# Kernel optimization log

Hardware: AMD Instinct MI355X
Metric: run time of the kernel (lower is better)

The kernel has to match this reference:

```python
import jax, jax.numpy as jnp
import numpy as np
import math

SIZE = 11
PAD = 5
C1 = 0.01 ** 2
C2 = 0.03 ** 2


def gaussian_window():
    # Matches torch __init__: 1D gaussian (sigma=1.5), normalized, outer product,
    # expanded to depthwise weight of shape (3, 1, 11, 11)
    x = np.arange(SIZE, dtype=np.float32)
    g = np.exp(-((x - SIZE // 2) ** 2) / (2.0 * 1.5 ** 2)).astype(np.float32)
    g = g / g.sum()
    w2d = np.outer(g, g).astype(np.float32)  # (11, 11)
    return jnp.asarray(np.broadcast_to(w2d, (3, 1, SIZE, SIZE)).copy())


def depthwise_conv(x, win):
    return jax.lax.conv_general_dilated(
        x, win,
        window_strides=(1, 1),
        padding=[(PAD, PAD), (PAD, PAD)],
        dimension_numbers=('NCHW', 'OIHW', 'NCHW'),
        feature_group_count=3,
    )


def setup_inputs() -> dict:
    key = jax.random.key(0)
    k1, k2 = jax.random.split(key)
    img1 = jax.random.uniform(k1, (16, 3, 512, 512), dtype=jnp.float32)
    img2 = jax.random.uniform(k2, (16, 3, 512, 512), dtype=jnp.float32)
    return {"img1": img1, "img2": img2, "win": gaussian_window()}


def reference(img1, img2, win):
    mu1 = depthwise_conv(img1, win)
    mu2 = depthwise_conv(img2, win)
    mu1_sq = mu1 * mu1
    mu2_sq = mu2 * mu2
    mu1_mu2 = mu1 * mu2
    sig1_sq = depthwise_conv(img1 * img1, win) - mu1_sq
    sig2_sq = depthwise_conv(img2 * img2, win) - mu2_sq
    sig12 = depthwise_conv(img1 * img2, win) - mu1_mu2
    v = ((2.0 * mu1_mu2 + C1) * (2.0 * sig12 + C2)) / (
        (mu1_sq + mu2_sq + C1) * (sig1_sq + sig2_sq + C2))
    return 1.0 - jnp.mean(v)
```

## Files before the change

kernel.cpp:

```cpp
#include <hip/hip_runtime.h>


#define IMG 512
#define NPIX (16LL * 3 * 512 * 512)
#define GX 8
#define GY 4
#define NG 8
#define NBLK (GX * GY * 48)
#define NPART NBLK

typedef short v8s __attribute__((ext_vector_type(8)));
typedef float v4f __attribute__((ext_vector_type(4)));
typedef __bf16 bf2 __attribute__((ext_vector_type(2)));
typedef float f2  __attribute__((ext_vector_type(2)));

static __device__ __forceinline__ int cvtpk2(f2 v) {
    bf2 r = __builtin_convertvector(v, bf2);
    return __builtin_bit_cast(int, r);
}
static __device__ __forceinline__ unsigned f2bf(float f) {
    unsigned u = __float_as_uint(f);
    return (u + 0x7FFFu + ((u >> 16) & 1u)) >> 16;
}

static __device__ __forceinline__ void gload16(const float* g, void* lds) {
    __builtin_amdgcn_global_load_lds(
        (const __attribute__((address_space(1))) void*)g,
        (__attribute__((address_space(3))) void*)lds, 16, 0, 0);
}

template <int N>
static __device__ __forceinline__ void vwait() {
    if constexpr (N == 8)      asm volatile("s_waitcnt vmcnt(8)" ::: "memory");
    else if constexpr (N == 4) asm volatile("s_waitcnt vmcnt(4)" ::: "memory");
    else                       asm volatile("s_waitcnt vmcnt(0)" ::: "memory");
    __builtin_amdgcn_sched_barrier(0);
}

static __device__ __forceinline__ void h_rt(
    const float4 (&L)[4], v8s band, short (*hw)[16][40], int lm, int quad, int slot)
{
    const v4f zacc = {0.f, 0.f, 0.f, 0.f};
    const float4 a0 = L[0], a1 = L[1], b0 = L[2], b1 = L[3];
    f2 a0l; a0l.x = a0.x; a0l.y = a0.y;   f2 a0h; a0h.x = a0.z; a0h.y = a0.w;
    f2 a1l; a1l.x = a1.x; a1l.y = a1.y;   f2 a1h; a1h.x = a1.z; a1h.y = a1.w;
    f2 b0l; b0l.x = b0.x; b0l.y = b0.y;   f2 b0h; b0h.x = b0.z; b0h.y = b0.w;
    f2 b1l; b1l.x = b1.x; b1l.y = b1.y;   f2 b1h; b1h.x = b1.z; b1h.y = b1.w;

    v8s A[4]; int4 w;
    w.x = cvtpk2(a0l); w.y = cvtpk2(a0h); w.z = cvtpk2(a1l); w.w = cvtpk2(a1h);
    A[0] = __builtin_bit_cast(v8s, w);
    w.x = cvtpk2(b0l); w.y = cvtpk2(b0h); w.z = cvtpk2(b1l); w.w = cvtpk2(b1h);
    A[1] = __builtin_bit_cast(v8s, w);
    w.x = cvtpk2(__builtin_elementwise_fma(a0l, a0l, b0l * b0l));
    w.y = cvtpk2(__builtin_elementwise_fma(a0h, a0h, b0h * b0h));
    w.z = cvtpk2(__builtin_elementwise_fma(a1l, a1l, b1l * b1l));
    w.w = cvtpk2(__builtin_elementwise_fma(a1h, a1h, b1h * b1h));
    A[2] = __builtin_bit_cast(v8s, w);
    w.x = cvtpk2(a0l * b0l); w.y = cvtpk2(a0h * b0h);
    w.z = cvtpk2(a1l * b1l); w.w = cvtpk2(a1h * b1h);
    A[3] = __builtin_bit_cast(v8s, w);

    #pragma unroll
    for (int p = 0; p < 4; ++p) {
        const v4f acc = __builtin_amdgcn_mfma_f32_16x16x32_bf16(A[p], band, zacc, 0, 0, 0);
        int2 w2;
        f2 lo; lo.x = acc[0]; lo.y = acc[1];
        f2 hi; hi.x = acc[2]; hi.y = acc[3];
        w2.x = cvtpk2(lo); w2.y = cvtpk2(hi);
        *(int2*)&hw[p][lm][slot * 16 + quad * 4] = w2;
    }
}

static __device__ __forceinline__ void v_t2(
    v8s band, short (*hw)[16][40], int lm, int quad, int o, f2& vsum)
{
    const v4f zacc = {0.f, 0.f, 0.f, 0.f};
    const int bs = (quad * 8 + o * 16) & 31;
    v4f acc[4];
    #pragma unroll
    for (int p = 0; p < 4; ++p) {
        const v8s hf = *(const v8s*)&hw[p][lm][bs];
        acc[p] = __builtin_amdgcn_mfma_f32_16x16x32_bf16(band, hf, zacc, 0, 0, 0);
    }
    const f2 C1v = {1e-4f, 1e-4f};
    const f2 C2v = {9e-4f, 9e-4f};
    const f2 two = {2.f, 2.f};
    #pragma unroll
    for (int h = 0; h < 2; ++h) {
        f2 m1; m1.x = acc[0][2 * h]; m1.y = acc[0][2 * h + 1];
        f2 m2; m2.x = acc[1][2 * h]; m2.y = acc[1][2 * h + 1];
        f2 es; es.x = acc[2][2 * h]; es.y = acc[2][2 * h + 1];
        f2 ex; ex.x = acc[3][2 * h]; ex.y = acc[3][2 * h + 1];
        const f2 m1s = m1 * m1, m2s = m2 * m2, m12 = m1 * m2;
        const f2 sig = es - m1s - m2s;
        const f2 s12 = ex - m12;
        const f2 num = __builtin_elementwise_fma(two, m12, C1v) *
                       __builtin_elementwise_fma(two, s12, C2v);
        const f2 den = (m1s + m2s + C1v) * (sig + C2v);
        f2 r; r.x = __builtin_amdgcn_rcpf(den.x); r.y = __builtin_amdgcn_rcpf(den.y);
        vsum = __builtin_elementwise_fma(num, r, vsum);
    }
}

__global__ __launch_bounds__(256, 2) void ssim_kernel(
    const float* __restrict__ img1,
    const float* __restrict__ img2,
    const float* __restrict__ win,
    float* __restrict__ partial)
{
    __shared__ __align__(16) short hb[4][4][16][40];
    __shared__ __align__(16) float4 raw[4][3][4][64];

    const int tid  = threadIdx.x;
    const int lane = tid & 63;
    const int wave = tid >> 6;
    const int lm   = lane & 15;
    const int quad = lane >> 4;

    const int bx = blockIdx.x, by = blockIdx.y, z = blockIdx.z;
    const int rowbase = by * (NG * 16);

    float gl = 0.f;
    if (lane < 11) gl = win[55 + lane] * rsqrtf(win[60]);
    v8s band;
    #pragma unroll
    for (int j = 0; j < 8; ++j) {
        const int t  = quad * 8 + j - lm - 3;
        const int tc = ((unsigned)t > 10u) ? 11 : t;
        band[j] = (short)f2bf(__shfl(gl, tc));
    }

    const size_t zoff = (size_t)z * IMG * IMG;
    const float* p1 = img1 + zoff;
    const float* p2 = img2 + zoff;

    const int gct = bx * 4 + wave;
    const bool colOK = (gct > 0) & (gct < 31);
    const int gcol = gct * 16 - 8 + quad * 8;
    const int  colA = gcol < 0 ? 0 : (gcol > IMG - 4 ? IMG - 4 : gcol);
    const int  colB = (gcol + 4) < 0 ? 0 : ((gcol + 4) > IMG - 4 ? IMG - 4 : (gcol + 4));
    const bool cbA  = (unsigned)gcol >= (unsigned)IMG;
    const bool cbB  = (unsigned)(gcol + 4) >= (unsigned)IMG;
    const bool topE = (by == 0), botE = (by == GY - 1);
    short (*hw)[16][40] = hb[wave];

    auto issue_g = [&](int k, int slot) {
        const int gr  = rowbase + k * 16 - 8 + lm;
        const int grc = gr < 0 ? 0 : (gr > IMG - 1 ? IMG - 1 : gr);
        const float* r1 = p1 + (size_t)grc * IMG;
        const float* r2 = p2 + (size_t)grc * IMG;
        gload16(r1 + colA, &raw[wave][slot][0][0]);
        gload16(r1 + colB, &raw[wave][slot][1][0]);
        gload16(r2 + colA, &raw[wave][slot][2][0]);
        gload16(r2 + colB, &raw[wave][slot][3][0]);
    };
    auto consume_h = [&](int k, int slot) {
        float4 L[4];
        L[0] = raw[wave][slot][0][lane];
        L[1] = raw[wave][slot][1][lane];
        L[2] = raw[wave][slot][2][lane];
        L[3] = raw[wave][slot][3][lane];
        const bool rowsE = (k == 0 && topE) || (k == NG && botE);
        if (!colOK || rowsE) {
            const int gr = rowbase + k * 16 - 8 + lm;
            const bool rbad = (unsigned)gr >= (unsigned)IMG;
            float4 zz; zz.x = zz.y = zz.z = zz.w = 0.f;
            if (rbad | cbA) { L[0] = zz; L[2] = zz; }
            if (rbad | cbB) { L[1] = zz; L[3] = zz; }
        }
        h_rt(L, band, hw, lm, quad, k & 1);
    };

    f2 vsum = {0.f, 0.f};
    issue_g(0, 0); issue_g(1, 1); issue_g(2, 2);
    vwait<8>(); consume_h(0, 0);
    issue_g(3, 0); vwait<8>(); consume_h(1, 1); v_t2(band, hw, lm, quad, 0, vsum);
    issue_g(4, 1); vwait<8>(); consume_h(2, 2); v_t2(band, hw, lm, quad, 1, vsum);
    issue_g(5, 2); vwait<8>(); consume_h(3, 0); v_t2(band, hw, lm, quad, 2, vsum);
    issue_g(6, 0); vwait<8>(); consume_h(4, 1); v_t2(band, hw, lm, quad, 3, vsum);
    issue_g(7, 1); vwait<8>(); consume_h(5, 2); v_t2(band, hw, lm, quad, 4, vsum);
    issue_g(8, 2); vwait<8>(); consume_h(6, 0); v_t2(band, hw, lm, quad, 5, vsum);
                   vwait<4>(); consume_h(7, 1); v_t2(band, hw, lm, quad, 6, vsum);
                   vwait<0>(); consume_h(8, 2); v_t2(band, hw, lm, quad, 7, vsum);

    float vs = vsum.x + vsum.y;
    #pragma unroll
    for (int off = 32; off > 0; off >>= 1)
        vs += __shfl_down(vs, off, 64);
    if (lane == 0) *(float*)&hb[wave][3][15][36] = vs;
    __syncthreads();
    if (tid == 0) {
        float t = 0.f;
        #pragma unroll
        for (int w = 0; w < 4; ++w) t += *(const float*)&hb[w][3][15][36];
        partial[(z * GY + by) * GX + bx] = t;
    }
}

__global__ __launch_bounds__(512) void finalize_kernel(
    const float* __restrict__ partial, float* __restrict__ out)
{
    __shared__ float red[8];
    float s = 0.f;
    if (threadIdx.x < NPART / 4) {
        const float4 t = ((const float4*)partial)[threadIdx.x];
        s = (t.x + t.y) + (t.z + t.w);
    }
    #pragma unroll
    for (int off = 32; off > 0; off >>= 1)
        s += __shfl_down(s, off, 64);
    if ((threadIdx.x & 63) == 0) red[threadIdx.x >> 6] = s;
    __syncthreads();
    if (threadIdx.x == 0) {
        float t = 0.f;
        #pragma unroll
        for (int i = 0; i < 8; ++i) t += red[i];
        out[0] = 1.0f - t / (float)NPIX;
    }
}

extern "C" void kernel_launch(void* const* d_in, const int* in_sizes, int n_in,
                              void* d_out, int out_size, void* d_ws, size_t ws_size,
                              hipStream_t stream) {
    const float* img1 = (const float*)d_in[0];
    const float* img2 = (const float*)d_in[1];
    const float* win  = (const float*)d_in[2];
    float* partialb = (float*)d_ws;

    dim3 grid(GX, GY, 48);
    ssim_kernel<<<grid, dim3(256), 0, stream>>>(img1, img2, win, partialb);
    finalize_kernel<<<1, dim3(512), 0, stream>>>(partialb, (float*)d_out);
}
```

Before: 136.8 us.

## Double-buffer global-to-LDS loads, lengthen row strips, and raise occupancy

Each block now covers 256 rows instead of 128 (GY 2, NG 16). This halves the redundant 16-row halo loads per strip. The triple-buffered raw LDS staging is replaced by a double buffer, with a looped schedule that reads the slot into registers before issuing the next load into it. The freed LDS and a launch bound of 3 blocks per SM are meant to raise occupancy. The tradeoffs are fewer blocks (768) to fill the GPU, shallower prefetch depth, and an extra lgkmcnt wait in each iteration.

```diff
diff --git a/kernel.cpp b/kernel.cpp
--- a/kernel.cpp
+++ b/kernel.cpp
@@ -4,8 +4,8 @@
 #define IMG 512
 #define NPIX (16LL * 3 * 512 * 512)
 #define GX 8
-#define GY 4
-#define NG 8
+#define GY 2
+#define NG 16
 #define NBLK (GX * GY * 48)
 #define NPART NBLK
 
@@ -31,9 +31,12 @@
 
 template <int N>
 static __device__ __forceinline__ void vwait() {
-    if constexpr (N == 8)      asm volatile("s_waitcnt vmcnt(8)" ::: "memory");
-    else if constexpr (N == 4) asm volatile("s_waitcnt vmcnt(4)" ::: "memory");
-    else                       asm volatile("s_waitcnt vmcnt(0)" ::: "memory");
+    if constexpr (N == 4) asm volatile("s_waitcnt vmcnt(4)" ::: "memory");
+    else                  asm volatile("s_waitcnt vmcnt(0)" ::: "memory");
+    __builtin_amdgcn_sched_barrier(0);
+}
+static __device__ __forceinline__ void lwait0() {
+    asm volatile("s_waitcnt lgkmcnt(0)" ::: "memory");
     __builtin_amdgcn_sched_barrier(0);
 }
 
@@ -103,14 +106,14 @@
     }
 }
 
-__global__ __launch_bounds__(256, 2) void ssim_kernel(
+__global__ __launch_bounds__(256, 3) void ssim_kernel(
     const float* __restrict__ img1,
     const float* __restrict__ img2,
     const float* __restrict__ win,
     float* __restrict__ partial)
 {
     __shared__ __align__(16) short hb[4][4][16][40];
-    __shared__ __align__(16) float4 raw[4][3][4][64];
+    __shared__ __align__(16) float4 raw[4][2][4][64];
 
     const int tid  = threadIdx.x;
     const int lane = tid & 63;
@@ -145,23 +148,23 @@
     const bool topE = (by == 0), botE = (by == GY - 1);
     short (*hw)[16][40] = hb[wave];
 
-    auto issue_g = [&](int k, int slot) {
+    auto issue_g = [&](int k) {
         const int gr  = rowbase + k * 16 - 8 + lm;
         const int grc = gr < 0 ? 0 : (gr > IMG - 1 ? IMG - 1 : gr);
         const float* r1 = p1 + (size_t)grc * IMG;
         const float* r2 = p2 + (size_t)grc * IMG;
-        gload16(r1 + colA, &raw[wave][slot][0][0]);
-        gload16(r1 + colB, &raw[wave][slot][1][0]);
-        gload16(r2 + colA, &raw[wave][slot][2][0]);
-        gload16(r2 + colB, &raw[wave][slot][3][0]);
+        void* s = &raw[wave][k & 1][0][0];
+        gload16(r1 + colA, s);
+        gload16(r1 + colB, (char*)s + 1024);
+        gload16(r2 + colA, (char*)s + 2048);
+        gload16(r2 + colB, (char*)s + 3072);
     };
-    auto consume_h = [&](int k, int slot) {
-        float4 L[4];
-        L[0] = raw[wave][slot][0][lane];
-        L[1] = raw[wave][slot][1][lane];
-        L[2] = raw[wave][slot][2][lane];
-        L[3] = raw[wave][slot][3][lane];
-        const bool rowsE = (k == 0 && topE) || (k == NG && botE);
+    auto read_g = [&](int k, float4 (&L)[4], bool rowsE) {
+        L[0] = raw[wave][k & 1][0][lane];
+        L[1] = raw[wave][k & 1][1][lane];
+        L[2] = raw[wave][k & 1][2][lane];
+        L[3] = raw[wave][k & 1][3][lane];
+        lwait0();
         if (!colOK || rowsE) {
             const int gr = rowbase + k * 16 - 8 + lm;
             const bool rbad = (unsigned)gr >= (unsigned)IMG;
@@ -169,20 +172,32 @@
             if (rbad | cbA) { L[0] = zz; L[2] = zz; }
             if (rbad | cbB) { L[1] = zz; L[3] = zz; }
         }
+    };
+
+    f2 vsum = {0.f, 0.f};
+    float4 L[4];
+
+    issue_g(0); issue_g(1);
+
+    vwait<4>(); read_g(0, L, topE);
+    issue_g(2);
+    h_rt(L, band, hw, lm, quad, 0);
+
+    #pragma unroll 2
+    for (int k = 1; k <= NG - 2; ++k) {
+        vwait<4>(); read_g(k, L, false);
+        issue_g(k + 2);
         h_rt(L, band, hw, lm, quad, k & 1);
-    };
-
-    f2 vsum = {0.f, 0.f};
-    issue_g(0, 0); issue_g(1, 1); issue_g(2, 2);
-    vwait<8>(); consume_h(0, 0);
-    issue_g(3, 0); vwait<8>(); consume_h(1, 1); v_t2(band, hw, lm, quad, 0, vsum);
-    issue_g(4, 1); vwait<8>(); consume_h(2, 2); v_t2(band, hw, lm, quad, 1, vsum);
-    issue_g(5, 2); vwait<8>(); consume_h(3, 0); v_t2(band, hw, lm, quad, 2, vsum);
-    issue_g(6, 0); vwait<8>(); consume_h(4, 1); v_t2(band, hw, lm, quad, 3, vsum);
-    issue_g(7, 1); vwait<8>(); consume_h(5, 2); v_t2(band, hw, lm, quad, 4, vsum);
-    issue_g(8, 2); vwait<8>(); consume_h(6, 0); v_t2(band, hw, lm, quad, 5, vsum);
-                   vwait<4>(); consume_h(7, 1); v_t2(band, hw, lm, quad, 6, vsum);
-                   vwait<0>(); consume_h(8, 2); v_t2(band, hw, lm, quad, 7, vsum);
+        v_t2(band, hw, lm, quad, k - 1, vsum);
+    }
+
+    vwait<4>(); read_g(NG - 1, L, false);
+    h_rt(L, band, hw, lm, quad, (NG - 1) & 1);
+    v_t2(band, hw, lm, quad, NG - 2, vsum);
+
+    vwait<0>(); read_g(NG, L, botE);
+    h_rt(L, band, hw, lm, quad, NG & 1);
+    v_t2(band, hw, lm, quad, NG - 1, vsum);
 
     float vs = vsum.x + vsum.y;
     #pragma unroll
```

New measurement: 141.0 us. +3.1%, slower.
